# Kernel tuning notes

Hardware: AMD Instinct MI355X
Metric: run time of the kernel (lower is better)

## Reference

```python
import jax, jax.numpy as jnp
import numpy as np
import math


def _dct_kernel():
    # Fixed 4x4 2D-DCT basis, 16 output filters, shape (16, 1, 4, 4) in OIHW.
    u = np.full(4, math.sqrt(2.0 / 4.0), dtype=np.float32)
    u[0] = math.sqrt(1.0 / 4.0)
    k = np.zeros((16, 1, 4, 4), dtype=np.float32)
    for kk in range(4):
        for ll in range(4):
            for i in range(4):
                for j in range(4):
                    k[kk * 4 + ll, 0, i, j] = (
                        u[kk] * u[ll]
                        * math.cos(math.pi / 8.0 * kk * (2 * i + 1))
                        * math.cos(math.pi / 8.0 * ll * (2 * j + 1))
                    )
    return jnp.asarray(k)


def setup_inputs() -> dict:
    key = jax.random.key(0)
    x = jax.random.normal(key, (8, 3, 512, 512), dtype=jnp.float32)
    return {"x": x}


def reference(x):
    B, C, H, W = x.shape
    dct = _dct_kernel()                       # (16, 1, 4, 4)
    kernel = jnp.tile(dct, (C, 1, 1, 1))      # (16*C, 1, 4, 4), grouped conv
    # Per-channel conv with the same fixed DCT kernel == grouped conv with
    # feature_group_count=C. padding=2 on a 4x4 kernel -> H+1, W+1 output.
    out = jax.lax.conv_general_dilated(
        x, kernel,
        window_strides=(1, 1),
        padding=[(2, 2), (2, 2)],
        dimension_numbers=("NCHW", "OIHW", "NCHW"),
        feature_group_count=C,
    )  # (B, 16*C, H+1, W+1)
    # DCT_Trunc(|out|) = -(relu(-|out|+8)-8) = min(|out|, 8)
    return jnp.minimum(jnp.abs(out), 8.0)
```

## Files before the change

### kernel.cpp

```cpp
#include <hip/hip_runtime.h>


#define IHW 512
#define OHW 513

__global__ __launch_bounds__(256) void dct_layer_kernel(
    const float* __restrict__ x, float* __restrict__ out) {
    const float A1 = 0.6532814824381883f;
    const float A2 = 0.2705980500730985f;

    int pix = blockIdx.x * 256 + threadIdx.x;
    if (pix >= OHW * OHW) return;
    int oh = pix / OHW;
    int ow = pix - oh * OHW;
    int bc = blockIdx.y;

    const float* __restrict__ xin = x + (size_t)bc * (IHW * IHW);

    float p[4][4];
#pragma unroll
    for (int i = 0; i < 4; ++i) {
        int ih = oh - 2 + i;
        bool rv = ((unsigned)ih < (unsigned)IHW);
        const float* row = xin + ih * IHW;
#pragma unroll
        for (int j = 0; j < 4; ++j) {
            int iw = ow - 2 + j;
            bool ok = rv && ((unsigned)iw < (unsigned)IHW);
            p[i][j] = ok ? row[iw] : 0.0f;
        }
    }

    float t[4][4];
#pragma unroll
    for (int j = 0; j < 4; ++j) {
        float s03 = p[0][j] + p[3][j];
        float d03 = p[0][j] - p[3][j];
        float s12 = p[1][j] + p[2][j];
        float d12 = p[1][j] - p[2][j];
        t[0][j] = 0.5f * (s03 + s12);
        t[1][j] = A1 * d03 + A2 * d12;
        t[2][j] = 0.5f * (s03 - s12);
        t[3][j] = A2 * d03 - A1 * d12;
    }

    float r[16];
#pragma unroll
    for (int kk = 0; kk < 4; ++kk) {
        float s03 = t[kk][0] + t[kk][3];
        float d03 = t[kk][0] - t[kk][3];
        float s12 = t[kk][1] + t[kk][2];
        float d12 = t[kk][1] - t[kk][2];
        r[kk * 4 + 0] = 0.5f * (s03 + s12);
        r[kk * 4 + 1] = A1 * d03 + A2 * d12;
        r[kk * 4 + 2] = 0.5f * (s03 - s12);
        r[kk * 4 + 3] = A2 * d03 - A1 * d12;
    }

    const size_t PLANE = (size_t)OHW * OHW;
    size_t obase = (size_t)bc * 16 * PLANE + (size_t)pix;
#pragma unroll
    for (int c = 0; c < 16; ++c) {
        out[obase + (size_t)c * PLANE] = fminf(fabsf(r[c]), 8.0f);
    }
}

extern "C" void kernel_launch(void* const* d_in, const int* in_sizes, int n_in,
                              void* d_out, int out_size, void* d_ws, size_t ws_size,
                              hipStream_t stream) {
    const float* x = (const float*)d_in[0];
    float* out = (float*)d_out;
    dim3 grid((OHW * OHW + 255) / 256, 24);
    hipLaunchKernelGGL(dct_layer_kernel, grid, dim3(256), 0, stream, x, out);
}
```

Baseline: 458.0 us.

## Split into interior and edge kernels, reuse row transforms across four output rows

Interior outputs run in a dedicated kernel with no bounds checks. Each thread computes four vertically adjacent output pixels, reusing seven horizontal row butterflies across them instead of recomputing them per pixel. Border pixels go to a separate small edge kernel that keeps the bounds-checked path. The kernel is dominated by output writes (about 200 MB), so the main gain would come from cutting load and compute overhead, at the cost of a second launch.

```diff
diff --git a/kernel.cpp b/kernel.cpp
--- a/kernel.cpp
+++ b/kernel.cpp
@@ -3,18 +3,86 @@
 
 #define IHW 512
 #define OHW 513
+#define PLANE ((size_t)OHW * (size_t)OHW)
 
-__global__ __launch_bounds__(256) void dct_layer_kernel(
-    const float* __restrict__ x, float* __restrict__ out) {
+__device__ __forceinline__ void bfly(float x0, float x1, float x2, float x3,
+                                     float& y0, float& y1, float& y2, float& y3) {
     const float A1 = 0.6532814824381883f;
     const float A2 = 0.2705980500730985f;
+    float s03 = x0 + x3, d03 = x0 - x3;
+    float s12 = x1 + x2, d12 = x1 - x2;
+    y0 = 0.5f * (s03 + s12);
+    y1 = A1 * d03 + A2 * d12;
+    y2 = 0.5f * (s03 - s12);
+    y3 = A2 * d03 - A1 * d12;
+}
 
-    int pix = blockIdx.x * 256 + threadIdx.x;
-    if (pix >= OHW * OHW) return;
-    int oh = pix / OHW;
-    int ow = pix - oh * OHW;
+__global__ __launch_bounds__(256) void dct_interior(const float* __restrict__ x,
+                                                    float* __restrict__ out) {
+    const int NT = 509 * 127;
+    int t = blockIdx.x * 256 + threadIdx.x;
+    if (t >= NT) return;
+    int s = t / 509;
+    int ow = 2 + (t - s * 509);
+    int oh0 = 2 + 4 * s;
     int bc = blockIdx.y;
 
+    const float* __restrict__ xin =
+        x + (size_t)bc * (IHW * IHW) + (size_t)(oh0 - 2) * IHW + (ow - 2);
+
+    float h[7][4];
+#pragma unroll
+    for (int i = 0; i < 7; ++i) {
+        float p0 = xin[i * IHW + 0];
+        float p1 = xin[i * IHW + 1];
+        float p2 = xin[i * IHW + 2];
+        float p3 = xin[i * IHW + 3];
+        bfly(p0, p1, p2, p3, h[i][0], h[i][1], h[i][2], h[i][3]);
+    }
+
+    size_t obase = (size_t)bc * 16 * PLANE + (size_t)oh0 * OHW + (size_t)ow;
+#pragma unroll
+    for (int o = 0; o < 4; ++o) {
+#pragma unroll
+        for (int ll = 0; ll < 4; ++ll) {
+            float v0, v1, v2, v3;
+            bfly(h[o][ll], h[o + 1][ll], h[o + 2][ll], h[o + 3][ll],
+                 v0, v1, v2, v3);
+            size_t a = obase + (size_t)o * OHW + (size_t)ll * PLANE;
+            out[a]              = fminf(fabsf(v0), 8.0f);
+            out[a + 4 * PLANE]  = fminf(fabsf(v1), 8.0f);
+            out[a + 8 * PLANE]  = fminf(fabsf(v2), 8.0f);
+            out[a + 12 * PLANE] = fminf(fabsf(v3), 8.0f);
+        }
+    }
+}
+
+__global__ __launch_bounds__(256) void dct_edge(const float* __restrict__ x,
+                                                float* __restrict__ out) {
+    const int NE = 4597;
+    int e = blockIdx.x * 256 + threadIdx.x;
+    if (e >= NE) return;
+    int oh, ow;
+    if (e < 1026) {
+        oh = (e >= 513) ? 1 : 0;
+        ow = e - oh * 513;
+    } else if (e < 2565) {
+        int f = e - 1026;
+        int r = f / 513;
+        oh = 510 + r;
+        ow = f - r * 513;
+    } else {
+        int f = e - 2565;
+        if (f < 1016) {
+            oh = 2 + (f >> 1);
+            ow = f & 1;
+        } else {
+            f -= 1016;
+            oh = 2 + (f >> 1);
+            ow = 511 + (f & 1);
+        }
+    }
+    int bc = blockIdx.y;
     const float* __restrict__ xin = x + (size_t)bc * (IHW * IHW);
 
     float p[4][4];
@@ -31,37 +99,20 @@
         }
     }
 
-    float t[4][4];
+    float h[4][4];
 #pragma unroll
-    for (int j = 0; j < 4; ++j) {
-        float s03 = p[0][j] + p[3][j];
-        float d03 = p[0][j] - p[3][j];
-        float s12 = p[1][j] + p[2][j];
-        float d12 = p[1][j] - p[2][j];
-        t[0][j] = 0.5f * (s03 + s12);
-        t[1][j] = A1 * d03 + A2 * d12;
-        t[2][j] = 0.5f * (s03 - s12);
-        t[3][j] = A2 * d03 - A1 * d12;
-    }
+    for (int i = 0; i < 4; ++i)
+        bfly(p[i][0], p[i][1], p[i][2], p[i][3], h[i][0], h[i][1], h[i][2], h[i][3]);
 
-    float r[16];
+    size_t obase = (size_t)bc * 16 * PLANE + (size_t)oh * OHW + (size_t)ow;
 #pragma unroll
-    for (int kk = 0; kk < 4; ++kk) {
-        float s03 = t[kk][0] + t[kk][3];
-        float d03 = t[kk][0] - t[kk][3];
-        float s12 = t[kk][1] + t[kk][2];
-        float d12 = t[kk][1] - t[kk][2];
-        r[kk * 4 + 0] = 0.5f * (s03 + s12);
-        r[kk * 4 + 1] = A1 * d03 + A2 * d12;
-        r[kk * 4 + 2] = 0.5f * (s03 - s12);
-        r[kk * 4 + 3] = A2 * d03 - A1 * d12;
-    }
-
-    const size_t PLANE = (size_t)OHW * OHW;
-    size_t obase = (size_t)bc * 16 * PLANE + (size_t)pix;
-#pragma unroll
-    for (int c = 0; c < 16; ++c) {
-        out[obase + (size_t)c * PLANE] = fminf(fabsf(r[c]), 8.0f);
+    for (int ll = 0; ll < 4; ++ll) {
+        float v0, v1, v2, v3;
+        bfly(h[0][ll], h[1][ll], h[2][ll], h[3][ll], v0, v1, v2, v3);
+        out[obase + (size_t)ll * PLANE]        = fminf(fabsf(v0), 8.0f);
+        out[obase + (size_t)(4 + ll) * PLANE]  = fminf(fabsf(v1), 8.0f);
+        out[obase + (size_t)(8 + ll) * PLANE]  = fminf(fabsf(v2), 8.0f);
+        out[obase + (size_t)(12 + ll) * PLANE] = fminf(fabsf(v3), 8.0f);
     }
 }
 
@@ -70,6 +121,10 @@
                               hipStream_t stream) {
     const float* x = (const float*)d_in[0];
     float* out = (float*)d_out;
-    dim3 grid((OHW * OHW + 255) / 256, 24);
-    hipLaunchKernelGGL(dct_layer_kernel, grid, dim3(256), 0, stream, x, out);
+
+    dim3 gi((509 * 127 + 255) / 256, 24);
+    hipLaunchKernelGGL(dct_interior, gi, dim3(256), 0, stream, x, out);
+
+    dim3 ge((4597 + 255) / 256, 24);
+    hipLaunchKernelGGL(dct_edge, ge, dim3(256), 0, stream, x, out);
 }
```

Result: slower. 496.1 us (+8.3%).

## Compute one DCT output plane per block with vertical row strips

Applied to the files above, without the earlier changes.

Each thread now produces a single DCT coefficient for a 16-row vertical strip at one column, instead of all 16 coefficients for one pixel. The grid covers all 384 output planes, so each block writes to one contiguous plane and the horizontal 4-tap result is reused across the strip's overlapping rows. The aim is to spread the write-bound output traffic over more blocks and cut per-pixel input loads. In exchange the input is re-read 16 times, once per coefficient plane, and the last strip overlaps the one before it and writes some rows twice.

```diff
diff --git a/kernel.cpp b/kernel.cpp
--- a/kernel.cpp
+++ b/kernel.cpp
@@ -3,65 +3,64 @@
 
 #define IHW 512
 #define OHW 513
+#define PLANE ((size_t)OHW * (size_t)OHW)
+#define RSTRIP 16
+#define NSTRIP 33
+#define JOB_T (513 * NSTRIP)
 
-__global__ __launch_bounds__(256) void dct_layer_kernel(
-    const float* __restrict__ x, float* __restrict__ out) {
+__global__ __launch_bounds__(256) void dct_plane(const float* __restrict__ x,
+                                                 float* __restrict__ out) {
     const float A1 = 0.6532814824381883f;
     const float A2 = 0.2705980500730985f;
 
-    int pix = blockIdx.x * 256 + threadIdx.x;
-    if (pix >= OHW * OHW) return;
-    int oh = pix / OHW;
-    int ow = pix - oh * OHW;
-    int bc = blockIdx.y;
+    int t = blockIdx.x * 256 + threadIdx.x;
+    if (t >= JOB_T) return;
+    int j = blockIdx.y;
+    int bc = j >> 4;
+    int kk = (j >> 2) & 3;
+    int ll = j & 3;
+
+    int s = t / 513;
+    int ow = t - s * 513;
+    int oh0 = s * RSTRIP;
+    if (oh0 > OHW - RSTRIP) oh0 = OHW - RSTRIP;
+
+    float g0 = (ll == 0) ? 0.5f : (ll == 1) ?  A1 : (ll == 2) ?  0.5f :  A2;
+    float g1 = (ll == 0) ? 0.5f : (ll == 1) ?  A2 : (ll == 2) ? -0.5f : -A1;
+    float g2 = (ll == 0) ? 0.5f : (ll == 1) ? -A2 : (ll == 2) ? -0.5f :  A1;
+    float g3 = (ll == 0) ? 0.5f : (ll == 1) ? -A1 : (ll == 2) ?  0.5f : -A2;
+    float c0 = (kk == 0) ? 0.5f : (kk == 1) ?  A1 : (kk == 2) ?  0.5f :  A2;
+    float c1 = (kk == 0) ? 0.5f : (kk == 1) ?  A2 : (kk == 2) ? -0.5f : -A1;
+    float c2 = (kk == 0) ? 0.5f : (kk == 1) ? -A2 : (kk == 2) ? -0.5f :  A1;
+    float c3 = (kk == 0) ? 0.5f : (kk == 1) ? -A1 : (kk == 2) ?  0.5f : -A2;
+
+    int iw0 = ow - 2;
+    int i0 = min(max(iw0,     0), IHW - 1);
+    int i1 = min(max(iw0 + 1, 0), IHW - 1);
+    int i2 = min(max(iw0 + 2, 0), IHW - 1);
+    int i3 = min(max(iw0 + 3, 0), IHW - 1);
+    float gm0 = ((unsigned)iw0       < (unsigned)IHW) ? g0 : 0.0f;
+    float gm1 = ((unsigned)(iw0 + 1) < (unsigned)IHW) ? g1 : 0.0f;
+    float gm2 = ((unsigned)(iw0 + 2) < (unsigned)IHW) ? g2 : 0.0f;
+    float gm3 = ((unsigned)(iw0 + 3) < (unsigned)IHW) ? g3 : 0.0f;
 
     const float* __restrict__ xin = x + (size_t)bc * (IHW * IHW);
 
-    float p[4][4];
+    float h[RSTRIP + 3];
 #pragma unroll
-    for (int i = 0; i < 4; ++i) {
-        int ih = oh - 2 + i;
-        bool rv = ((unsigned)ih < (unsigned)IHW);
-        const float* row = xin + ih * IHW;
-#pragma unroll
-        for (int j = 0; j < 4; ++j) {
-            int iw = ow - 2 + j;
-            bool ok = rv && ((unsigned)iw < (unsigned)IHW);
-            p[i][j] = ok ? row[iw] : 0.0f;
-        }
+    for (int i = 0; i < RSTRIP + 3; ++i) {
+        int ih = oh0 - 2 + i;
+        int ihc = min(max(ih, 0), IHW - 1);
+        const float* __restrict__ row = xin + ihc * IHW;
+        float v = gm0 * row[i0] + gm1 * row[i1] + gm2 * row[i2] + gm3 * row[i3];
+        h[i] = ((unsigned)ih < (unsigned)IHW) ? v : 0.0f;
     }
 
-    float t[4][4];
+    float* __restrict__ op = out + (size_t)j * PLANE + (size_t)oh0 * OHW + ow;
 #pragma unroll
-    for (int j = 0; j < 4; ++j) {
-        float s03 = p[0][j] + p[3][j];
-        float d03 = p[0][j] - p[3][j];
-        float s12 = p[1][j] + p[2][j];
-        float d12 = p[1][j] - p[2][j];
-        t[0][j] = 0.5f * (s03 + s12);
-        t[1][j] = A1 * d03 + A2 * d12;
-        t[2][j] = 0.5f * (s03 - s12);
-        t[3][j] = A2 * d03 - A1 * d12;
-    }
-
-    float r[16];
-#pragma unroll
-    for (int kk = 0; kk < 4; ++kk) {
-        float s03 = t[kk][0] + t[kk][3];
-        float d03 = t[kk][0] - t[kk][3];
-        float s12 = t[kk][1] + t[kk][2];
-        float d12 = t[kk][1] - t[kk][2];
-        r[kk * 4 + 0] = 0.5f * (s03 + s12);
-        r[kk * 4 + 1] = A1 * d03 + A2 * d12;
-        r[kk * 4 + 2] = 0.5f * (s03 - s12);
-        r[kk * 4 + 3] = A2 * d03 - A1 * d12;
-    }
-
-    const size_t PLANE = (size_t)OHW * OHW;
-    size_t obase = (size_t)bc * 16 * PLANE + (size_t)pix;
-#pragma unroll
-    for (int c = 0; c < 16; ++c) {
-        out[obase + (size_t)c * PLANE] = fminf(fabsf(r[c]), 8.0f);
+    for (int o = 0; o < RSTRIP; ++o) {
+        float v = c0 * h[o] + c1 * h[o + 1] + c2 * h[o + 2] + c3 * h[o + 3];
+        op[(size_t)o * OHW] = fminf(fabsf(v), 8.0f);
     }
 }
 
@@ -70,6 +69,6 @@
                               hipStream_t stream) {
     const float* x = (const float*)d_in[0];
     float* out = (float*)d_out;
-    dim3 grid((OHW * OHW + 255) / 256, 24);
-    hipLaunchKernelGGL(dct_layer_kernel, grid, dim3(256), 0, stream, x, out);
+    dim3 grid((JOB_T + 255) / 256, 384);
+    hipLaunchKernelGGL(dct_plane, grid, dim3(256), 0, stream, x, out);
 }
```

After: 626.7 us. +36.8%, slower.

## Tile output rows per block with LDS-staged input and separable DCT reuse

Applied to the files above, without the earlier changes.

Each block now covers a strip of 4 output rows across the full width. It stages the 7 needed input rows in shared memory, using float4 loads for interior strips, and computes the horizontal 1D DCT once per input row, reusing it across the overlapping output rows. This removes the redundant 16 global loads per output pixel and the repeated horizontal transforms. The last strip is clamped to overlap the previous one, so some rows are computed and written twice. A single thread handles the extra last column, which adds serial tail work. The kernel is output-write bound (about 400MB written), so the gains may be limited.

```diff
diff --git a/kernel.cpp b/kernel.cpp
--- a/kernel.cpp
+++ b/kernel.cpp
@@ -3,65 +3,139 @@
 
 #define IHW 512
 #define OHW 513
+#define PLANE ((size_t)OHW * (size_t)OHW)
+#define RS 4
+#define NS 129
+#define XW 520
 
-__global__ __launch_bounds__(256) void dct_layer_kernel(
-    const float* __restrict__ x, float* __restrict__ out) {
+__global__ __launch_bounds__(256) void dct_v5(const float* __restrict__ x,
+                                              float* __restrict__ out) {
     const float A1 = 0.6532814824381883f;
     const float A2 = 0.2705980500730985f;
 
-    int pix = blockIdx.x * 256 + threadIdx.x;
-    if (pix >= OHW * OHW) return;
-    int oh = pix / OHW;
-    int ow = pix - oh * OHW;
-    int bc = blockIdx.y;
+    __shared__ float xs[7 * XW];
 
-    const float* __restrict__ xin = x + (size_t)bc * (IHW * IHW);
+    const int t = threadIdx.x;
+    const int bc = blockIdx.y;
+    int r0 = blockIdx.x * RS;
+    if (r0 > OHW - RS) r0 = OHW - RS;
 
-    float p[4][4];
+    const float* __restrict__ xin = x + (size_t)bc * ((size_t)IHW * IHW);
+
+    if (r0 >= 2 && r0 + RS <= IHW - 1) {
+        const float4* __restrict__ src = (const float4*)(xin + (size_t)(r0 - 2) * IHW);
 #pragma unroll
-    for (int i = 0; i < 4; ++i) {
-        int ih = oh - 2 + i;
-        bool rv = ((unsigned)ih < (unsigned)IHW);
-        const float* row = xin + ih * IHW;
+        for (int k = 0; k < 4; ++k) {
+            int idx = t + k * 256;
+            if (idx < 896) {
+                float4 v = src[idx];
+                int f = idx << 2;
+                int i = f >> 9;
+                int c = f & 511;
+                float* d = &xs[i * XW + 4 + c];
+                d[0] = v.x; d[1] = v.y; d[2] = v.z; d[3] = v.w;
+            }
+        }
+    } else {
 #pragma unroll
-        for (int j = 0; j < 4; ++j) {
-            int iw = ow - 2 + j;
-            bool ok = rv && ((unsigned)iw < (unsigned)IHW);
-            p[i][j] = ok ? row[iw] : 0.0f;
+        for (int i = 0; i < 7; ++i) {
+            int ih = r0 - 2 + i;
+            bool rv = (unsigned)ih < (unsigned)IHW;
+            const float* __restrict__ row = xin + (size_t)(rv ? ih : 0) * IHW;
+#pragma unroll
+            for (int k = 0; k < 2; ++k) {
+                int c = t + k * 256;
+                float v = row[c];
+                xs[i * XW + 4 + c] = rv ? v : 0.0f;
+            }
+        }
+    }
+    if (t < 7) {
+        xs[t * XW + 2]   = 0.0f;
+        xs[t * XW + 3]   = 0.0f;
+        xs[t * XW + 516] = 0.0f;
+        xs[t * XW + 517] = 0.0f;
+    }
+    __syncthreads();
+
+    float h0[4][7], h1[4][7];
+#pragma unroll
+    for (int i = 0; i < 7; ++i) {
+        const float* __restrict__ r = &xs[i * XW + 2 + t];
+        {
+            float v0 = r[0], v1 = r[1], v2 = r[2], v3 = r[3];
+            float s03 = v0 + v3, d03 = v0 - v3, s12 = v1 + v2, d12 = v1 - v2;
+            h0[0][i] = 0.5f * (s03 + s12);
+            h0[1][i] = A1 * d03 + A2 * d12;
+            h0[2][i] = 0.5f * (s03 - s12);
+            h0[3][i] = A2 * d03 - A1 * d12;
+        }
+        {
+            float v0 = r[256], v1 = r[257], v2 = r[258], v3 = r[259];
+            float s03 = v0 + v3, d03 = v0 - v3, s12 = v1 + v2, d12 = v1 - v2;
+            h1[0][i] = 0.5f * (s03 + s12);
+            h1[1][i] = A1 * d03 + A2 * d12;
+            h1[2][i] = 0.5f * (s03 - s12);
+            h1[3][i] = A2 * d03 - A1 * d12;
         }
     }
 
-    float t[4][4];
+    const size_t oc = (size_t)bc * 16 * PLANE + (size_t)r0 * OHW;
 #pragma unroll
-    for (int j = 0; j < 4; ++j) {
-        float s03 = p[0][j] + p[3][j];
-        float d03 = p[0][j] - p[3][j];
-        float s12 = p[1][j] + p[2][j];
-        float d12 = p[1][j] - p[2][j];
-        t[0][j] = 0.5f * (s03 + s12);
-        t[1][j] = A1 * d03 + A2 * d12;
-        t[2][j] = 0.5f * (s03 - s12);
-        t[3][j] = A2 * d03 - A1 * d12;
+    for (int o = 0; o < RS; ++o) {
+        size_t rowoff = oc + (size_t)o * OHW;
+#pragma unroll
+        for (int ll = 0; ll < 4; ++ll) {
+            float s03a = h0[ll][o] + h0[ll][o + 3], d03a = h0[ll][o] - h0[ll][o + 3];
+            float s12a = h0[ll][o + 1] + h0[ll][o + 2], d12a = h0[ll][o + 1] - h0[ll][o + 2];
+            float s03b = h1[ll][o] + h1[ll][o + 3], d03b = h1[ll][o] - h1[ll][o + 3];
+            float s12b = h1[ll][o + 1] + h1[ll][o + 2], d12b = h1[ll][o + 1] - h1[ll][o + 2];
+
+            float ua0 = 0.5f * (s03a + s12a), ub0 = 0.5f * (s03b + s12b);
+            float ua1 = A1 * d03a + A2 * d12a, ub1 = A1 * d03b + A2 * d12b;
+            float ua2 = 0.5f * (s03a - s12a), ub2 = 0.5f * (s03b - s12b);
+            float ua3 = A2 * d03a - A1 * d12a, ub3 = A2 * d03b - A1 * d12b;
+
+            out[rowoff + (size_t)(0 * 4 + ll) * PLANE + t]       = fminf(fabsf(ua0), 8.0f);
+            out[rowoff + (size_t)(0 * 4 + ll) * PLANE + t + 256] = fminf(fabsf(ub0), 8.0f);
+            out[rowoff + (size_t)(1 * 4 + ll) * PLANE + t]       = fminf(fabsf(ua1), 8.0f);
+            out[rowoff + (size_t)(1 * 4 + ll) * PLANE + t + 256] = fminf(fabsf(ub1), 8.0f);
+            out[rowoff + (size_t)(2 * 4 + ll) * PLANE + t]       = fminf(fabsf(ua2), 8.0f);
+            out[rowoff + (size_t)(2 * 4 + ll) * PLANE + t + 256] = fminf(fabsf(ub2), 8.0f);
+            out[rowoff + (size_t)(3 * 4 + ll) * PLANE + t]       = fminf(fabsf(ua3), 8.0f);
+            out[rowoff + (size_t)(3 * 4 + ll) * PLANE + t + 256] = fminf(fabsf(ub3), 8.0f);
+        }
     }
 
-    float r[16];
+    if (t == 0) {
+        float h2[4][7];
 #pragma unroll
-    for (int kk = 0; kk < 4; ++kk) {
-        float s03 = t[kk][0] + t[kk][3];
-        float d03 = t[kk][0] - t[kk][3];
-        float s12 = t[kk][1] + t[kk][2];
-        float d12 = t[kk][1] - t[kk][2];
-        r[kk * 4 + 0] = 0.5f * (s03 + s12);
-        r[kk * 4 + 1] = A1 * d03 + A2 * d12;
-        r[kk * 4 + 2] = 0.5f * (s03 - s12);
-        r[kk * 4 + 3] = A2 * d03 - A1 * d12;
-    }
-
-    const size_t PLANE = (size_t)OHW * OHW;
-    size_t obase = (size_t)bc * 16 * PLANE + (size_t)pix;
+        for (int i = 0; i < 7; ++i) {
+            float v0 = xs[i * XW + 514], v1 = xs[i * XW + 515];
+            float v2 = xs[i * XW + 516], v3 = xs[i * XW + 517];
+            float s03 = v0 + v3, d03 = v0 - v3, s12 = v1 + v2, d12 = v1 - v2;
+            h2[0][i] = 0.5f * (s03 + s12);
+            h2[1][i] = A1 * d03 + A2 * d12;
+            h2[2][i] = 0.5f * (s03 - s12);
+            h2[3][i] = A2 * d03 - A1 * d12;
+        }
 #pragma unroll
-    for (int c = 0; c < 16; ++c) {
-        out[obase + (size_t)c * PLANE] = fminf(fabsf(r[c]), 8.0f);
+        for (int o = 0; o < RS; ++o) {
+#pragma unroll
+            for (int ll = 0; ll < 4; ++ll) {
+                float s03 = h2[ll][o] + h2[ll][o + 3], d03 = h2[ll][o] - h2[ll][o + 3];
+                float s12 = h2[ll][o + 1] + h2[ll][o + 2], d12 = h2[ll][o + 1] - h2[ll][o + 2];
+                float u0 = 0.5f * (s03 + s12);
+                float u1 = A1 * d03 + A2 * d12;
+                float u2 = 0.5f * (s03 - s12);
+                float u3 = A2 * d03 - A1 * d12;
+                size_t rowoff = oc + (size_t)o * OHW + 512;
+                out[rowoff + (size_t)(0 * 4 + ll) * PLANE] = fminf(fabsf(u0), 8.0f);
+                out[rowoff + (size_t)(1 * 4 + ll) * PLANE] = fminf(fabsf(u1), 8.0f);
+                out[rowoff + (size_t)(2 * 4 + ll) * PLANE] = fminf(fabsf(u2), 8.0f);
+                out[rowoff + (size_t)(3 * 4 + ll) * PLANE] = fminf(fabsf(u3), 8.0f);
+            }
+        }
     }
 }
 
@@ -70,6 +144,6 @@
                               hipStream_t stream) {
     const float* x = (const float*)d_in[0];
     float* out = (float*)d_out;
-    dim3 grid((OHW * OHW + 255) / 256, 24);
-    hipLaunchKernelGGL(dct_layer_kernel, grid, dim3(256), 0, stream, x, out);
+    dim3 grid(NS, 24);
+    hipLaunchKernelGGL(dct_v5, grid, dim3(256), 0, stream, x, out);
 }
```

New measurement: 472.6 us. 1.03x slower.
